# Optimization experiments

Hardware: AMD Instinct MI355X
Metric: run time of the kernel (lower is better)

## Reference

```python
import jax, jax.numpy as jnp
import numpy as np

H = 1024
NH = 16
HD = H // NH  # 64

def setup_inputs() -> dict:
    key = jax.random.key(0)
    ks = jax.random.split(key, 6)
    B, S = 2, 2048
    hidden_states = jax.random.normal(ks[0], (B, S, H), dtype=jnp.float32)
    attention_mask = jnp.ones((B, S), dtype=jnp.int32)
    sc = 1.0 / np.sqrt(H)
    Wq = jax.random.normal(ks[1], (H, H), dtype=jnp.float32) * sc
    Wk = jax.random.normal(ks[2], (H, H), dtype=jnp.float32) * sc
    Wv = jax.random.normal(ks[3], (H, H), dtype=jnp.float32) * sc
    Wo = jax.random.normal(ks[4], (H, H), dtype=jnp.float32) * sc
    return {"hidden_states": hidden_states, "attention_mask": attention_mask,
            "Wq": Wq, "Wk": Wk, "Wv": Wv, "Wo": Wo}

def reference(hidden_states, attention_mask, Wq, Wk, Wv, Wo):
    B, S, _ = hidden_states.shape
    # nn.Linear(bias=False): y = x @ W.T
    q = hidden_states @ Wq.T
    k = hidden_states @ Wk.T
    v = hidden_states @ Wv.T
    # [B, NH, S, HD]
    q = q.reshape(B, S, NH, HD).transpose(0, 2, 1, 3)
    k = k.reshape(B, S, NH, HD).transpose(0, 2, 1, 3)
    v = v.reshape(B, S, NH, HD).transpose(0, 2, 1, 3)
    # ELU+1 feature map
    q = jax.nn.elu(q) + 1.0
    k = jax.nn.elu(k) + 1.0
    # [B, NH, S, S]
    attn = jnp.einsum('bhqd,bhkd->bhqk', q, k)
    mask = attention_mask[:, None, None, :]  # [B,1,1,S]
    attn = jnp.where(mask == 0, -jnp.inf, attn)
    attn = jax.nn.softmax(attn, axis=-1)
    # dropout p=0.0 (eval) -> identity
    out = jnp.einsum('bhqk,bhkd->bhqd', attn, v)
    out = out.transpose(0, 2, 1, 3).reshape(B, S, H)
    return out @ Wo.T
```

## Files before the change

kernel.cpp:

```cpp
#include <hip/hip_runtime.h>

#define H_ 1024
#define NH_ 16
#define HD_ 64
#define B_ 2
#define S_ 2048
#define BS_ 4096

typedef _Float16 half8 __attribute__((ext_vector_type(8)));
typedef _Float16 half4_t __attribute__((ext_vector_type(4)));
typedef float floatx4 __attribute__((ext_vector_type(4)));

#define LOG2E 1.44269504088896f

__device__ __forceinline__ void async_copy16(void* lds, const void* g) {
  __builtin_amdgcn_global_load_lds(
      (const __attribute__((address_space(1))) unsigned int*)g,
      (__attribute__((address_space(3))) unsigned int*)lds, 16, 0, 0);
}

__global__ __launch_bounds__(256) void cvt_all(
    const float* __restrict__ hs, const float* __restrict__ wq,
    const float* __restrict__ wk, const float* __restrict__ wv,
    const float* __restrict__ wo,
    _Float16* __restrict__ hs_h, _Float16* __restrict__ w_h) {
  int i = blockIdx.x * 256 + threadIdx.x;
  int idx = i * 4;
  const float* src; _Float16* dst; int off;
  if (idx < BS_ * H_) {
    src = hs; dst = hs_h; off = idx;
  } else {
    int j = idx - BS_ * H_;
    int w = j >> 20;
    off = j & ((1 << 20) - 1);
    src = (w == 0) ? wq : (w == 1) ? wk : (w == 2) ? wv : wo;
    dst = w_h + (size_t)w * (H_ * H_);
  }
  float4 f = *(const float4*)(src + off);
  half4_t o;
  o.x = (_Float16)f.x; o.y = (_Float16)f.y;
  o.z = (_Float16)f.z; o.w = (_Float16)f.w;
  *(half4_t*)(dst + off) = o;
}

__global__ __launch_bounds__(256, 3) void qkv_gemm(
    const _Float16* __restrict__ A, const _Float16* __restrict__ Wall,
    _Float16* __restrict__ qh, _Float16* __restrict__ kh,
    _Float16* __restrict__ vt) {
  const int d = blockIdx.x;
  const int y = d & 31;
  const int k = d >> 5;
  const int x = k & 7;
  const int z = k >> 3;
  const _Float16* W = Wall + (size_t)z * (H_ * H_);
  const int rbase = y * 128;
  const int cbase = x * 128;
  __shared__ _Float16 SM[24576];
  const int tid = threadIdx.x, lane = tid & 63, w = tid >> 6;
  const int quad = lane >> 4, l16 = lane & 15;
  const int wr = (w >> 1) * 64, wc = (w & 1) * 64;

  floatx4 zero = {0.f, 0.f, 0.f, 0.f};
  floatx4 acc[4][4];
#pragma unroll
  for (int i = 0; i < 4; ++i)
#pragma unroll
    for (int j = 0; j < 4; ++j) acc[i][j] = zero;

  const int srow = tid >> 2;
  const int pslot = tid & 3;
  const int sslot = pslot ^ ((srow >> 1) & 3);
  const _Float16* Ag = A + (size_t)(rbase + srow) * H_ + sslot * 8;
  const _Float16* Bg = W + (size_t)(cbase + srow) * H_ + sslot * 8;

  auto STAGE = [&](int s, int t) {
    const int k0 = t * 32;
    _Float16* ab = &SM[s * 4096 + tid * 8];
    _Float16* bb = &SM[12288 + s * 4096 + tid * 8];
    async_copy16(ab, Ag + k0);
    async_copy16(ab + 2048, Ag + (size_t)64 * H_ + k0);
    async_copy16(bb, Bg + k0);
    async_copy16(bb + 2048, Bg + (size_t)64 * H_ + k0);
  };

  const int rsw = (l16 >> 1) & 3;
  auto COMPUTE = [&](int s) {
    const _Float16* Ap = &SM[s * 4096];
    const _Float16* Bp = &SM[12288 + s * 4096];
    half8 af[4], bf[4];
#pragma unroll
    for (int t = 0; t < 4; ++t)
      af[t] = *(const half8*)&Ap[(wr + t * 16 + l16) * 32 + (quad ^ rsw) * 8];
#pragma unroll
    for (int t = 0; t < 4; ++t)
      bf[t] = *(const half8*)&Bp[(wc + t * 16 + l16) * 32 + (quad ^ rsw) * 8];
    __builtin_amdgcn_s_setprio(1);
#pragma unroll
    for (int i = 0; i < 4; ++i)
#pragma unroll
      for (int j = 0; j < 4; ++j)
        acc[i][j] = __builtin_amdgcn_mfma_f32_16x16x32_f16(af[i], bf[j],
                                                           acc[i][j], 0, 0, 0);
    __builtin_amdgcn_s_setprio(0);
  };

  STAGE(0, 0);
  STAGE(1, 1);
  int sc = 0;
  for (int t = 0; t < 30; ++t) {
    asm volatile("s_waitcnt vmcnt(4)" ::: "memory");
    __builtin_amdgcn_sched_barrier(0);
    __builtin_amdgcn_s_barrier();
    __builtin_amdgcn_sched_barrier(0);
    int ss = sc + 2; if (ss >= 3) ss -= 3;
    STAGE(ss, t + 2);
    COMPUTE(sc);
    sc = (sc == 2) ? 0 : sc + 1;
  }
  asm volatile("s_waitcnt vmcnt(4)" ::: "memory");
  __builtin_amdgcn_sched_barrier(0);
  __builtin_amdgcn_s_barrier();
  __builtin_amdgcn_sched_barrier(0);
  COMPUTE(sc);
  sc = (sc == 2) ? 0 : sc + 1;
  asm volatile("s_waitcnt vmcnt(0)" ::: "memory");
  __builtin_amdgcn_sched_barrier(0);
  __builtin_amdgcn_s_barrier();
  __builtin_amdgcn_sched_barrier(0);
  COMPUTE(sc);

  __syncthreads();
  const int PAD = 132;
  const int b = rbase >> 11, sl_base = rbase & (S_ - 1);
  if (z != 2) {
    const float scale = (z == 0) ? LOG2E : 1.0f;
#pragma unroll
    for (int i = 0; i < 4; ++i) {
      int s0 = wr + i * 16 + quad * 4;
#pragma unroll
      for (int j = 0; j < 4; ++j) {
        int c = wc + j * 16 + l16;
#pragma unroll
        for (int r = 0; r < 4; ++r) {
          float xx = acc[i][j][r];
          xx = ((xx > 0.f) ? (xx + 1.f) : __expf(xx)) * scale;
          SM[(s0 + r) * PAD + c] = (_Float16)xx;
        }
      }
    }
    __syncthreads();
    _Float16* outp = (z == 0) ? qh : kh;
#pragma unroll
    for (int k2 = 0; k2 < 8; ++k2) {
      int c2 = tid + k2 * 256;
      int s = c2 >> 4, part = c2 & 15;
      int col = cbase + part * 8;
      int h = col >> 6, dd = col & 63;
      half8 vvv = *(const half8*)&SM[s * PAD + part * 8];
      *(half8*)&outp[((size_t)(b * NH_ + h) * S_ + sl_base + s) * HD_ + dd] = vvv;
    }
  } else {
#pragma unroll
    for (int i = 0; i < 4; ++i) {
      int s0 = wr + i * 16 + quad * 4;
#pragma unroll
      for (int j = 0; j < 4; ++j) {
        int c = wc + j * 16 + l16;
#pragma unroll
        for (int r = 0; r < 4; ++r)
          SM[c * PAD + s0 + r] = (_Float16)acc[i][j][r];
      }
    }
    __syncthreads();
#pragma unroll
    for (int k2 = 0; k2 < 8; ++k2) {
      int c2 = tid + k2 * 256;
      int c = c2 >> 4, part = c2 & 15;
      int col = cbase + c;
      int h = col >> 6, dd = col & 63;
      half8 vvv = *(const half8*)&SM[c * PAD + part * 8];
      *(half8*)&vt[((size_t)(b * NH_ + h) * HD_ + dd) * S_ + sl_base + part * 8] = vvv;
    }
  }
}

__global__ __launch_bounds__(256, 2) void flash_attn(
    const _Float16* __restrict__ qh, const _Float16* __restrict__ kh,
    const _Float16* __restrict__ vt, const int* __restrict__ mask,
    _Float16* __restrict__ attn_out) {
  const int dd = blockIdx.x;
  const int bh = dd & 31, b = bh >> 4, h = bh & 15;
  const int qbase = (dd >> 5) * 128;
  const int tid = threadIdx.x, w = tid >> 6, lane = tid & 63;
  const int quad = lane >> 4, l16 = lane & 15;

  __shared__ _Float16 Kt[2][128 * 64];
  __shared__ _Float16 Vt[2][64 * 128];

  const _Float16* Q = qh + (size_t)bh * (S_ * HD_);
  const _Float16* K = kh + (size_t)bh * (S_ * HD_);
  const _Float16* Vg = vt + (size_t)bh * (HD_ * S_);
  const int* Mb = mask + b * S_;

  half8 qf[2][2];
#pragma unroll
  for (int g = 0; g < 2; ++g) {
    int qr = qbase + w * 32 + g * 16 + l16;
    qf[g][0] = *(const half8*)&Q[qr * 64 + quad * 8];
    qf[g][1] = *(const half8*)&Q[qr * 64 + 32 + quad * 8];
  }

  floatx4 zero = {0.f, 0.f, 0.f, 0.f};
  floatx4 o[2][4];
#pragma unroll
  for (int g = 0; g < 2; ++g)
#pragma unroll
    for (int i = 0; i < 4; ++i) o[g][i] = zero;
  float mi[2] = {-3e38f, -3e38f}, li[2] = {0.f, 0.f};

  const int krow_off = lane >> 3;
  const int kslot = lane & 7;
  const int kchunk = kslot ^ (krow_off & 7);
  const int vrow_off = lane >> 4;
  const int vslot = lane & 15;

  {
#pragma unroll
    for (int u = 0; u < 4; ++u) {
      int kl = w * 32 + u * 8;
      async_copy16(&Kt[0][kl * 64], K + (size_t)(kl + krow_off) * 64 + kchunk * 8);
    }
#pragma unroll
    for (int u = 0; u < 4; ++u) {
      int d0 = w * 16 + u * 4 + vrow_off;
      int c0 = vslot ^ (d0 & 15);
      async_copy16(&Vt[0][(w * 16 + u * 4) * 128], Vg + (size_t)d0 * S_ + c0 * 8);
    }
  }

  for (int kt = 0; kt < S_ / 128; ++kt) {
    const int key0 = kt * 128;
    const int buf = kt & 1;
    __syncthreads();
    if (kt < S_ / 128 - 1) {
      const int key1 = key0 + 128;
#pragma unroll
      for (int u = 0; u < 4; ++u) {
        int kl = w * 32 + u * 8;
        async_copy16(&Kt[buf ^ 1][kl * 64],
                     K + (size_t)(key1 + kl + krow_off) * 64 + kchunk * 8);
      }
#pragma unroll
      for (int u = 0; u < 4; ++u) {
        int d0 = w * 16 + u * 4 + vrow_off;
        int c0 = vslot ^ (d0 & 15);
        async_copy16(&Vt[buf ^ 1][(w * 16 + u * 4) * 128],
                     Vg + (size_t)d0 * S_ + key1 + c0 * 8);
      }
    }
    int m0 = Mb[key0 + lane];
    int m1 = Mb[key0 + 64 + lane];

    const _Float16* Kb = &Kt[buf][0];
    const _Float16* Vb = &Vt[buf][0];

    floatx4 sa[2][8];
#pragma unroll
    for (int g = 0; g < 2; ++g)
#pragma unroll
      for (int ct = 0; ct < 8; ++ct) sa[g][ct] = zero;
    {
      int s0 = quad ^ (l16 & 7);
      int s1 = (4 + quad) ^ (l16 & 7);
#pragma unroll
      for (int ct = 0; ct < 8; ++ct) {
        int key = ct * 16 + l16;
        half8 bf0 = *(half8*)&Kb[key * 64 + s0 * 8];
        half8 bf1 = *(half8*)&Kb[key * 64 + s1 * 8];
        sa[0][ct] = __builtin_amdgcn_mfma_f32_16x16x32_f16(bf0, qf[0][0], sa[0][ct], 0, 0, 0);
        sa[0][ct] = __builtin_amdgcn_mfma_f32_16x16x32_f16(bf1, qf[0][1], sa[0][ct], 0, 0, 0);
        sa[1][ct] = __builtin_amdgcn_mfma_f32_16x16x32_f16(bf0, qf[1][0], sa[1][ct], 0, 0, 0);
        sa[1][ct] = __builtin_amdgcn_mfma_f32_16x16x32_f16(bf1, qf[1][1], sa[1][ct], 0, 0, 0);
      }
    }
    if (__any((m0 == 0) || (m1 == 0))) {
#pragma unroll
      for (int ct = 0; ct < 8; ++ct)
#pragma unroll
        for (int r = 0; r < 4; ++r)
          if (Mb[key0 + ct * 16 + quad * 4 + r] == 0) {
            sa[0][ct][r] = -1e30f;
            sa[1][ct][r] = -1e30f;
          }
    }
#pragma unroll
    for (int g = 0; g < 2; ++g) {
      float mx = sa[g][0][0];
#pragma unroll
      for (int ct = 0; ct < 8; ++ct)
#pragma unroll
        for (int r = 0; r < 4; ++r) mx = fmaxf(mx, sa[g][ct][r]);
      mx = fmaxf(mx, __shfl_xor(mx, 16));
      mx = fmaxf(mx, __shfl_xor(mx, 32));
      float mn = fmaxf(mi[g], mx);
      float alpha = __builtin_amdgcn_exp2f(mi[g] - mn);
      mi[g] = mn;
      float rs = 0.f;
#pragma unroll
      for (int ct = 0; ct < 8; ++ct)
#pragma unroll
        for (int r = 0; r < 4; ++r) {
          float p = __builtin_amdgcn_exp2f(sa[g][ct][r] - mn);
          sa[g][ct][r] = p;
          rs += p;
        }
      rs += __shfl_xor(rs, 16);
      rs += __shfl_xor(rs, 32);
      li[g] = li[g] * alpha + rs;
#pragma unroll
      for (int ct2 = 0; ct2 < 4; ++ct2) {
        o[g][ct2][0] *= alpha; o[g][ct2][1] *= alpha;
        o[g][ct2][2] *= alpha; o[g][ct2][3] *= alpha;
      }
    }
#pragma unroll
    for (int ct = 0; ct < 8; ++ct) {
      half4_t p0, p1;
#pragma unroll
      for (int r = 0; r < 4; ++r) {
        p0[r] = (_Float16)sa[0][ct][r];
        p1[r] = (_Float16)sa[1][ct][r];
      }
      int chunk = (2 * ct + (quad >> 1)) ^ l16;
      int off = chunk * 8 + (quad & 1) * 4;
#pragma unroll
      for (int ct2 = 0; ct2 < 4; ++ct2) {
        int dx = ct2 * 16 + l16;
        half4_t vf = *(half4_t*)&Vb[dx * 128 + off];
        o[0][ct2] = __builtin_amdgcn_mfma_f32_16x16x16f16(vf, p0, o[0][ct2], 0, 0, 0);
        o[1][ct2] = __builtin_amdgcn_mfma_f32_16x16x16f16(vf, p1, o[1][ct2], 0, 0, 0);
      }
    }
  }
#pragma unroll
  for (int g = 0; g < 2; ++g) {
    float inv = 1.0f / li[g];
    int row = qbase + w * 32 + g * 16 + l16;
#pragma unroll
    for (int ct2 = 0; ct2 < 4; ++ct2) {
      half4_t pk;
#pragma unroll
      for (int r = 0; r < 4; ++r) pk[r] = (_Float16)(o[g][ct2][r] * inv);
      int dx = ct2 * 16 + quad * 4;
      *(half4_t*)&attn_out[((size_t)(b * S_ + row)) * H_ + h * HD_ + dx] = pk;
    }
  }
}

__global__ __launch_bounds__(256, 2) void out_gemm(
    const _Float16* __restrict__ A, const _Float16* __restrict__ W,
    float* __restrict__ out) {
  const int d = blockIdx.x;
  const int y = d & 31;
  const int x = d >> 5;
  const int rbase = y * 128;
  const int cbase = x * 64;
  __shared__ _Float16 SM[36864];
  const int tid = threadIdx.x, lane = tid & 63, w = tid >> 6;
  const int quad = lane >> 4, l16 = lane & 15;

  floatx4 zero = {0.f, 0.f, 0.f, 0.f};
  floatx4 acc[2][4];
#pragma unroll
  for (int i = 0; i < 2; ++i)
#pragma unroll
    for (int j = 0; j < 4; ++j) acc[i][j] = zero;

  const int srow = tid >> 3;
  const int pslot = tid & 7;
  const int sslot = pslot ^ (srow & 7);
  const _Float16* Ag = A + (size_t)(rbase + srow) * H_ + sslot * 8;
  const _Float16* Bg = W + (size_t)(cbase + srow) * H_ + sslot * 8;

  auto STAGE = [&](int s, int t) {
    const int k0 = t * 64;
    _Float16* ab = &SM[s * 8192 + tid * 8];
    _Float16* bb = &SM[24576 + s * 4096 + tid * 8];
#pragma unroll
    for (int u = 0; u < 4; ++u)
      async_copy16(ab + u * 2048, Ag + (size_t)(u * 32) * H_ + k0);
#pragma unroll
    for (int u = 0; u < 2; ++u)
      async_copy16(bb + u * 2048, Bg + (size_t)(u * 32) * H_ + k0);
  };

  const int rsw = l16 & 7;
  auto COMPUTE = [&](int s) {
    const _Float16* Ap = &SM[s * 8192];
    const _Float16* Bp = &SM[24576 + s * 4096];
    half8 af[2][2], bf[4][2];
#pragma unroll
    for (int i = 0; i < 2; ++i)
#pragma unroll
      for (int hh = 0; hh < 2; ++hh)
        af[i][hh] = *(const half8*)&Ap[(w * 32 + i * 16 + l16) * 64 +
                                       (((hh * 4 + quad) ^ rsw) * 8)];
#pragma unroll
    for (int j = 0; j < 4; ++j)
#pragma unroll
      for (int hh = 0; hh < 2; ++hh)
        bf[j][hh] = *(const half8*)&Bp[(j * 16 + l16) * 64 +
                                       (((hh * 4 + quad) ^ rsw) * 8)];
    __builtin_amdgcn_s_setprio(1);
#pragma unroll
    for (int i = 0; i < 2; ++i)
#pragma unroll
      for (int j = 0; j < 4; ++j) {
        acc[i][j] = __builtin_amdgcn_mfma_f32_16x16x32_f16(af[i][0], bf[j][0],
                                                           acc[i][j], 0, 0, 0);
        acc[i][j] = __builtin_amdgcn_mfma_f32_16x16x32_f16(af[i][1], bf[j][1],
                                                           acc[i][j], 0, 0, 0);
      }
    __builtin_amdgcn_s_setprio(0);
  };

  STAGE(0, 0);
  STAGE(1, 1);
  int sc = 0;
  for (int t = 0; t < 14; ++t) {
    asm volatile("s_waitcnt vmcnt(6)" ::: "memory");
    __builtin_amdgcn_sched_barrier(0);
    __builtin_amdgcn_s_barrier();
    __builtin_amdgcn_sched_barrier(0);
    int ss = sc + 2; if (ss >= 3) ss -= 3;
    STAGE(ss, t + 2);
    COMPUTE(sc);
    sc = (sc == 2) ? 0 : sc + 1;
  }
  asm volatile("s_waitcnt vmcnt(6)" ::: "memory");
  __builtin_amdgcn_sched_barrier(0);
  __builtin_amdgcn_s_barrier();
  __builtin_amdgcn_sched_barrier(0);
  COMPUTE(sc);
  sc = (sc == 2) ? 0 : sc + 1;
  asm volatile("s_waitcnt vmcnt(0)" ::: "memory");
  __builtin_amdgcn_sched_barrier(0);
  __builtin_amdgcn_s_barrier();
  __builtin_amdgcn_sched_barrier(0);
  COMPUTE(sc);

  __syncthreads();
  float* FB = (float*)SM;
  const int FPAD = 68;
#pragma unroll
  for (int i = 0; i < 2; ++i) {
    int s0 = w * 32 + i * 16 + quad * 4;
#pragma unroll
    for (int j = 0; j < 4; ++j) {
      int c = j * 16 + l16;
#pragma unroll
      for (int r = 0; r < 4; ++r)
        FB[(s0 + r) * FPAD + c] = acc[i][j][r];
    }
  }
  __syncthreads();
#pragma unroll
  for (int k2 = 0; k2 < 8; ++k2) {
    int c2 = tid + k2 * 256;
    int s = c2 >> 4, part = c2 & 15;
    *(float4*)&out[(size_t)(rbase + s) * H_ + cbase + part * 4] =
        *(float4*)&FB[s * FPAD + part * 4];
  }
}

extern "C" void kernel_launch(void* const* d_in, const int* in_sizes, int n_in,
                              void* d_out, int out_size, void* d_ws,
                              size_t ws_size, hipStream_t stream) {
  const float* hs = (const float*)d_in[0];
  const int* mask = (const int*)d_in[1];
  const float* Wq = (const float*)d_in[2];
  const float* Wk = (const float*)d_in[3];
  const float* Wv = (const float*)d_in[4];
  const float* Wo = (const float*)d_in[5];
  float* out = (float*)d_out;

  _Float16* p = (_Float16*)d_ws;
  _Float16* hs_h = p; p += (size_t)BS_ * H_;
  _Float16* w_h = p;  p += (size_t)4 * H_ * H_;
  _Float16* q_h = p;  p += (size_t)BS_ * H_;
  _Float16* k_h = p;  p += (size_t)BS_ * H_;
  _Float16* v_t = p;  p += (size_t)BS_ * H_;
  _Float16* ao_h = p; p += (size_t)BS_ * H_;

  cvt_all<<<8192, 256, 0, stream>>>(hs, Wq, Wk, Wv, Wo, hs_h, w_h);
  qkv_gemm<<<768, 256, 0, stream>>>(hs_h, w_h, q_h, k_h, v_t);
  flash_attn<<<512, 256, 0, stream>>>(q_h, k_h, v_t, mask, ao_h);
  out_gemm<<<512, 256, 0, stream>>>(ao_h, w_h + (size_t)3 * H_ * H_, out);
}
```

Before: 189.3 us.

## Fuse fp32-to-fp16 conversion into GEMM loads and drop separate convert kernel

Removes the standalone conversion kernel and has the QKV and output GEMMs read fp32 inputs and weights directly, converting them to fp16 in registers before writing to LDS. The pipeline changes from a three-stage async global-to-LDS copy to a register-staged double buffer (load next tile to registers, convert, store to LDS). This saves one launch plus the fp16 write and reread of the activations and weights. In exchange the GEMMs read twice as many bytes from fp32 sources, lose the direct-to-LDS async copies, and have a shallower prefetch.

```diff
diff --git a/kernel.cpp b/kernel.cpp
--- a/kernel.cpp
+++ b/kernel.cpp
@@ -19,32 +19,18 @@
       (__attribute__((address_space(3))) unsigned int*)lds, 16, 0, 0);
 }
 
-__global__ __launch_bounds__(256) void cvt_all(
-    const float* __restrict__ hs, const float* __restrict__ wq,
-    const float* __restrict__ wk, const float* __restrict__ wv,
-    const float* __restrict__ wo,
-    _Float16* __restrict__ hs_h, _Float16* __restrict__ w_h) {
-  int i = blockIdx.x * 256 + threadIdx.x;
-  int idx = i * 4;
-  const float* src; _Float16* dst; int off;
-  if (idx < BS_ * H_) {
-    src = hs; dst = hs_h; off = idx;
-  } else {
-    int j = idx - BS_ * H_;
-    int w = j >> 20;
-    off = j & ((1 << 20) - 1);
-    src = (w == 0) ? wq : (w == 1) ? wk : (w == 2) ? wv : wo;
-    dst = w_h + (size_t)w * (H_ * H_);
-  }
-  float4 f = *(const float4*)(src + off);
-  half4_t o;
-  o.x = (_Float16)f.x; o.y = (_Float16)f.y;
-  o.z = (_Float16)f.z; o.w = (_Float16)f.w;
-  *(half4_t*)(dst + off) = o;
+__device__ __forceinline__ half8 cvt8(float4 lo, float4 hi) {
+  half8 h;
+  h[0] = (_Float16)lo.x; h[1] = (_Float16)lo.y;
+  h[2] = (_Float16)lo.z; h[3] = (_Float16)lo.w;
+  h[4] = (_Float16)hi.x; h[5] = (_Float16)hi.y;
+  h[6] = (_Float16)hi.z; h[7] = (_Float16)hi.w;
+  return h;
 }
 
 __global__ __launch_bounds__(256, 3) void qkv_gemm(
-    const _Float16* __restrict__ A, const _Float16* __restrict__ Wall,
+    const float* __restrict__ A, const float* __restrict__ Wq,
+    const float* __restrict__ Wk, const float* __restrict__ Wv,
     _Float16* __restrict__ qh, _Float16* __restrict__ kh,
     _Float16* __restrict__ vt) {
   const int d = blockIdx.x;
@@ -52,10 +38,10 @@
   const int k = d >> 5;
   const int x = k & 7;
   const int z = k >> 3;
-  const _Float16* W = Wall + (size_t)z * (H_ * H_);
+  const float* W = (z == 0) ? Wq : (z == 1) ? Wk : Wv;
   const int rbase = y * 128;
   const int cbase = x * 128;
-  __shared__ _Float16 SM[24576];
+  __shared__ _Float16 SM[16896];
   const int tid = threadIdx.x, lane = tid & 63, w = tid >> 6;
   const int quad = lane >> 4, l16 = lane & 15;
   const int wr = (w >> 1) * 64, wc = (w & 1) * 64;
@@ -70,23 +56,34 @@
   const int srow = tid >> 2;
   const int pslot = tid & 3;
   const int sslot = pslot ^ ((srow >> 1) & 3);
-  const _Float16* Ag = A + (size_t)(rbase + srow) * H_ + sslot * 8;
-  const _Float16* Bg = W + (size_t)(cbase + srow) * H_ + sslot * 8;
-
-  auto STAGE = [&](int s, int t) {
+  const float* Ag = A + (size_t)(rbase + srow) * H_ + sslot * 8;
+  const float* Bg = W + (size_t)(cbase + srow) * H_ + sslot * 8;
+
+  float4 ra[4], rb[4];
+  auto LOAD = [&](int t) {
     const int k0 = t * 32;
+    ra[0] = *(const float4*)(Ag + k0);
+    ra[1] = *(const float4*)(Ag + k0 + 4);
+    ra[2] = *(const float4*)(Ag + (size_t)64 * H_ + k0);
+    ra[3] = *(const float4*)(Ag + (size_t)64 * H_ + k0 + 4);
+    rb[0] = *(const float4*)(Bg + k0);
+    rb[1] = *(const float4*)(Bg + k0 + 4);
+    rb[2] = *(const float4*)(Bg + (size_t)64 * H_ + k0);
+    rb[3] = *(const float4*)(Bg + (size_t)64 * H_ + k0 + 4);
+  };
+  auto WRITE = [&](int s) {
     _Float16* ab = &SM[s * 4096 + tid * 8];
-    _Float16* bb = &SM[12288 + s * 4096 + tid * 8];
-    async_copy16(ab, Ag + k0);
-    async_copy16(ab + 2048, Ag + (size_t)64 * H_ + k0);
-    async_copy16(bb, Bg + k0);
-    async_copy16(bb + 2048, Bg + (size_t)64 * H_ + k0);
+    _Float16* bb = &SM[8192 + s * 4096 + tid * 8];
+    *(half8*)ab = cvt8(ra[0], ra[1]);
+    *(half8*)(ab + 2048) = cvt8(ra[2], ra[3]);
+    *(half8*)bb = cvt8(rb[0], rb[1]);
+    *(half8*)(bb + 2048) = cvt8(rb[2], rb[3]);
   };
 
   const int rsw = (l16 >> 1) & 3;
   auto COMPUTE = [&](int s) {
     const _Float16* Ap = &SM[s * 4096];
-    const _Float16* Bp = &SM[12288 + s * 4096];
+    const _Float16* Bp = &SM[8192 + s * 4096];
     half8 af[4], bf[4];
 #pragma unroll
     for (int t = 0; t < 4; ++t)
@@ -104,30 +101,16 @@
     __builtin_amdgcn_s_setprio(0);
   };
 
-  STAGE(0, 0);
-  STAGE(1, 1);
-  int sc = 0;
-  for (int t = 0; t < 30; ++t) {
-    asm volatile("s_waitcnt vmcnt(4)" ::: "memory");
-    __builtin_amdgcn_sched_barrier(0);
+  LOAD(0);
+  for (int t = 0; t < 32; ++t) {
+    __syncthreads();
+    WRITE(t & 1);
+    if (t < 31) LOAD(t + 1);
+    asm volatile("s_waitcnt lgkmcnt(0)" ::: "memory");
     __builtin_amdgcn_s_barrier();
     __builtin_amdgcn_sched_barrier(0);
-    int ss = sc + 2; if (ss >= 3) ss -= 3;
-    STAGE(ss, t + 2);
-    COMPUTE(sc);
-    sc = (sc == 2) ? 0 : sc + 1;
-  }
-  asm volatile("s_waitcnt vmcnt(4)" ::: "memory");
-  __builtin_amdgcn_sched_barrier(0);
-  __builtin_amdgcn_s_barrier();
-  __builtin_amdgcn_sched_barrier(0);
-  COMPUTE(sc);
-  sc = (sc == 2) ? 0 : sc + 1;
-  asm volatile("s_waitcnt vmcnt(0)" ::: "memory");
-  __builtin_amdgcn_sched_barrier(0);
-  __builtin_amdgcn_s_barrier();
-  __builtin_amdgcn_sched_barrier(0);
-  COMPUTE(sc);
+    COMPUTE(t & 1);
+  }
 
   __syncthreads();
   const int PAD = 132;
@@ -358,14 +341,14 @@
 }
 
 __global__ __launch_bounds__(256, 2) void out_gemm(
-    const _Float16* __restrict__ A, const _Float16* __restrict__ W,
+    const _Float16* __restrict__ A, const float* __restrict__ W,
     float* __restrict__ out) {
   const int d = blockIdx.x;
   const int y = d & 31;
   const int x = d >> 5;
   const int rbase = y * 128;
   const int cbase = x * 64;
-  __shared__ _Float16 SM[36864];
+  __shared__ _Float16 SM[24576];
   const int tid = threadIdx.x, lane = tid & 63, w = tid >> 6;
   const int quad = lane >> 4, l16 = lane & 15;
 
@@ -380,24 +363,33 @@
   const int pslot = tid & 7;
   const int sslot = pslot ^ (srow & 7);
   const _Float16* Ag = A + (size_t)(rbase + srow) * H_ + sslot * 8;
-  const _Float16* Bg = W + (size_t)(cbase + srow) * H_ + sslot * 8;
-
-  auto STAGE = [&](int s, int t) {
+  const float* Bg = W + (size_t)(cbase + srow) * H_ + sslot * 8;
+
+  half8 qa[4];
+  float4 rb[4];
+  auto LOAD = [&](int t) {
     const int k0 = t * 64;
+#pragma unroll
+    for (int u = 0; u < 4; ++u)
+      qa[u] = *(const half8*)(Ag + (size_t)(u * 32) * H_ + k0);
+    rb[0] = *(const float4*)(Bg + k0);
+    rb[1] = *(const float4*)(Bg + k0 + 4);
+    rb[2] = *(const float4*)(Bg + (size_t)32 * H_ + k0);
+    rb[3] = *(const float4*)(Bg + (size_t)32 * H_ + k0 + 4);
+  };
+  auto WRITE = [&](int s) {
     _Float16* ab = &SM[s * 8192 + tid * 8];
-    _Float16* bb = &SM[24576 + s * 4096 + tid * 8];
-#pragma unroll
-    for (int u = 0; u < 4; ++u)
-      async_copy16(ab + u * 2048, Ag + (size_t)(u * 32) * H_ + k0);
-#pragma unroll
-    for (int u = 0; u < 2; ++u)
-      async_copy16(bb + u * 2048, Bg + (size_t)(u * 32) * H_ + k0);
+    _Float16* bb = &SM[16384 + s * 4096 + tid * 8];
+#pragma unroll
+    for (int u = 0; u < 4; ++u) *(half8*)(ab + u * 2048) = qa[u];
+    *(half8*)bb = cvt8(rb[0], rb[1]);
+    *(half8*)(bb + 2048) = cvt8(rb[2], rb[3]);
   };
 
   const int rsw = l16 & 7;
   auto COMPUTE = [&](int s) {
     const _Float16* Ap = &SM[s * 8192];
-    const _Float16* Bp = &SM[24576 + s * 4096];
+    const _Float16* Bp = &SM[16384 + s * 4096];
     half8 af[2][2], bf[4][2];
 #pragma unroll
     for (int i = 0; i < 2; ++i)
@@ -424,30 +416,16 @@
     __builtin_amdgcn_s_setprio(0);
   };
 
-  STAGE(0, 0);
-  STAGE(1, 1);
-  int sc = 0;
-  for (int t = 0; t < 14; ++t) {
-    asm volatile("s_waitcnt vmcnt(6)" ::: "memory");
-    __builtin_amdgcn_sched_barrier(0);
+  LOAD(0);
+  for (int t = 0; t < 16; ++t) {
+    __syncthreads();
+    WRITE(t & 1);
+    if (t < 15) LOAD(t + 1);
+    asm volatile("s_waitcnt lgkmcnt(0)" ::: "memory");
     __builtin_amdgcn_s_barrier();
     __builtin_amdgcn_sched_barrier(0);
-    int ss = sc + 2; if (ss >= 3) ss -= 3;
-    STAGE(ss, t + 2);
-    COMPUTE(sc);
-    sc = (sc == 2) ? 0 : sc + 1;
-  }
-  asm volatile("s_waitcnt vmcnt(6)" ::: "memory");
-  __builtin_amdgcn_sched_barrier(0);
-  __builtin_amdgcn_s_barrier();
-  __builtin_amdgcn_sched_barrier(0);
-  COMPUTE(sc);
-  sc = (sc == 2) ? 0 : sc + 1;
-  asm volatile("s_waitcnt vmcnt(0)" ::: "memory");
-  __builtin_amdgcn_sched_barrier(0);
-  __builtin_amdgcn_s_barrier();
-  __builtin_amdgcn_sched_barrier(0);
-  COMPUTE(sc);
+    COMPUTE(t & 1);
+  }
 
   __syncthreads();
   float* FB = (float*)SM;
@@ -485,15 +463,12 @@
   float* out = (float*)d_out;
 
   _Float16* p = (_Float16*)d_ws;
-  _Float16* hs_h = p; p += (size_t)BS_ * H_;
-  _Float16* w_h = p;  p += (size_t)4 * H_ * H_;
   _Float16* q_h = p;  p += (size_t)BS_ * H_;
   _Float16* k_h = p;  p += (size_t)BS_ * H_;
   _Float16* v_t = p;  p += (size_t)BS_ * H_;
   _Float16* ao_h = p; p += (size_t)BS_ * H_;
 
-  cvt_all<<<8192, 256, 0, stream>>>(hs, Wq, Wk, Wv, Wo, hs_h, w_h);
-  qkv_gemm<<<768, 256, 0, stream>>>(hs_h, w_h, q_h, k_h, v_t);
+  qkv_gemm<<<768, 256, 0, stream>>>(hs, Wq, Wk, Wv, q_h, k_h, v_t);
   flash_attn<<<512, 256, 0, stream>>>(q_h, k_h, v_t, mask, ao_h);
-  out_gemm<<<512, 256, 0, stream>>>(ao_h, w_h + (size_t)3 * H_ * H_, out);
-}
+  out_gemm<<<512, 256, 0, stream>>>(ao_h, Wo, out);
+}
```

New measurement: 189.7 us. Within noise of the previous version (+0.2%).
